# Kernel optimization log

Measured on AMD Instinct MI355X. Metric: run time of the kernel, lower is better.

The kernel has to match this reference:

```python
import jax, jax.numpy as jnp
import numpy as np

RESOLUTION = 0.1  # init arg `resolution`; hard=True -> hardtanh branch


def setup_inputs() -> dict:
    key = jax.random.key(0)
    B, L = 32, 1024  # documents x sentences per document
    score = jax.random.normal(key, (B * L,), dtype=jnp.float32)
    score_idx = jnp.arange(B * L, dtype=jnp.int32).reshape(B, L)
    return {"score": score, "score_idx": score_idx}


def _toeplitz(s):
    # Equivalent of pad_score: rows i = n-1 .. 1 of concat(zeros(n), s)
    # score_hat[r, j] = s[j - 1 - r] if j - 1 - r >= 0 else 0
    n = s.shape[0]
    r = jnp.arange(n - 1)[:, None]
    j = jnp.arange(n)[None, :]
    idx = j - 1 - r
    return jnp.where(idx >= 0, s[jnp.clip(idx, 0)], jnp.zeros((), s.dtype))


def _prob(score_hat, s):
    # hard=True: (hardtanh((hat - s)/res * 2 + 1) + 1) / 2
    z = (score_hat - s[None, :]) / RESOLUTION * 2.0 + 1.0
    return (jnp.clip(z, -1.0, 1.0) + 1.0) * 0.5


def _gate(s_doc):
    s = s_doc[1:-1]  # drop first/last sentence scores, length n = L-2
    fwd = jnp.cumprod(_prob(_toeplitz(s), s), axis=0)   # [n-1, n]
    sb = s[::-1]
    bwd = jnp.cumprod(_prob(_toeplitz(sb), sb), axis=0)  # [n-1, n]
    return jnp.stack([fwd, bwd], axis=0)  # [2, n-1, n]


def reference(score, score_idx):
    docs = score[score_idx]          # [B, L] gather per score_idx
    return jax.vmap(_gate)(docs)     # [B, 2, L-3, L-2]
```

## Files before the change

### kernel.cpp

```cpp
#include <hip/hip_runtime.h>

#define TPB   128
#define LSEQ  1024
#define NCOL  1022
#define NROW  1021
#define NPAD  1021
#define SLDS  (NPAD + NCOL)

__global__ __launch_bounds__(TPB) void gate_kernel(
    const float* __restrict__ score,
    const int*   __restrict__ score_idx,
    float*       __restrict__ out)
{
    __shared__ float sp[SLDS];

    const int bid = blockIdx.x;
    const int cb  = bid & 7;
    const int bd  = bid >> 3;
    const int d   = bd & 1;
    const int b   = bd >> 1;
    const int tid = threadIdx.x;

    for (int i = tid; i < NPAD; i += TPB) sp[i] = 0.0f;
    const int* idxRow = score_idx + b * LSEQ + 1;
    for (int i = tid; i < NCOL; i += TPB) {
        int src = (d == 0) ? i : (NCOL - 1 - i);
        sp[NPAD + i] = score[idxRow[src]];
    }
    __syncthreads();

    const int j = cb * TPB + tid;
    if (j >= NCOL) return;

    const float c = 1.0f - 10.0f * sp[NPAD + j];
    float a = 1.0f;
    int   m = NPAD + j - 1;
    float* outp = out + (size_t)bd * NROW * NCOL + j;

#define ROW(X)                                                        \
    {   float p = fminf(fmaxf(__builtin_fmaf((X), 10.0f, c), 0.0f), 1.0f); \
        a *= p; *outp = a; outp += NCOL; }

    for (int bt = 0; bt < NROW / 8; ++bt) {
        float x0 = sp[m    ], x1 = sp[m - 1], x2 = sp[m - 2], x3 = sp[m - 3];
        float x4 = sp[m - 4], x5 = sp[m - 5], x6 = sp[m - 6], x7 = sp[m - 7];
        m -= 8;
        ROW(x0); ROW(x1); ROW(x2); ROW(x3);
        ROW(x4); ROW(x5); ROW(x6); ROW(x7);
    }
    {
        float x0 = sp[m], x1 = sp[m - 1], x2 = sp[m - 2], x3 = sp[m - 3];
        float x4 = sp[m - 4];
        ROW(x0); ROW(x1); ROW(x2); ROW(x3); ROW(x4);
    }
#undef ROW
}

extern "C" void kernel_launch(void* const* d_in, const int* in_sizes, int n_in,
                              void* d_out, int out_size, void* d_ws, size_t ws_size,
                              hipStream_t stream)
{
    const float* score = (const float*)d_in[0];
    const int*   sidx  = (const int*)d_in[1];
    float*       out   = (float*)d_out;

    const int B = in_sizes[0] / LSEQ;
    dim3 grid(B * 2 * 8), block(TPB);
    gate_kernel<<<grid, block, 0, stream>>>(score, sidx, out);
}
```

Before: 50.87 us.

## Split work by row chunks with two columns per thread and paired stores

Each block now covers all columns for a 128-row slice of the cumulative product, instead of 128 columns across all rows. Each thread handles two adjacent columns and stores both as one 8-byte vector, so a block writes whole contiguous rows. Every thread first recomputes the running product up to its chunk's starting row, which adds redundant ALU and LDS work that grows for later chunks. The aim is better store coalescing and vector width on this write-bound kernel.

```diff
diff --git a/kernel.cpp b/kernel.cpp
--- a/kernel.cpp
+++ b/kernel.cpp
@@ -1,11 +1,15 @@
 #include <hip/hip_runtime.h>
 
-#define TPB   128
-#define LSEQ  1024
-#define NCOL  1022
-#define NROW  1021
-#define NPAD  1021
-#define SLDS  (NPAD + NCOL)
+#define TPB     512
+#define LSEQ    1024
+#define NCOL    1022
+#define NROW    1021
+#define NPAD    1021
+#define SLDS    (NPAD + NCOL)
+#define NCHUNK  8
+#define RPC     128
+
+typedef float v2f __attribute__((ext_vector_type(2)));
 
 __global__ __launch_bounds__(TPB) void gate_kernel(
     const float* __restrict__ score,
@@ -14,12 +18,12 @@
 {
     __shared__ float sp[SLDS];
 
-    const int bid = blockIdx.x;
-    const int cb  = bid & 7;
-    const int bd  = bid >> 3;
-    const int d   = bd & 1;
-    const int b   = bd >> 1;
-    const int tid = threadIdx.x;
+    const int bid   = blockIdx.x;
+    const int chunk = bid & (NCHUNK - 1);
+    const int bd    = bid >> 3;
+    const int d     = bd & 1;
+    const int b     = bd >> 1;
+    const int tid   = threadIdx.x;
 
     for (int i = tid; i < NPAD; i += TPB) sp[i] = 0.0f;
     const int* idxRow = score_idx + b * LSEQ + 1;
@@ -29,31 +33,54 @@
     }
     __syncthreads();
 
-    const int j = cb * TPB + tid;
-    if (j >= NCOL) return;
+    const int j0 = tid * 2;
+    if (j0 >= NCOL) return;
 
-    const float c = 1.0f - 10.0f * sp[NPAD + j];
-    float a = 1.0f;
-    int   m = NPAD + j - 1;
-    float* outp = out + (size_t)bd * NROW * NCOL + j;
+    const float c0 = 1.0f - 10.0f * sp[NPAD + j0];
+    const float c1 = 1.0f - 10.0f * sp[NPAD + j0 + 1];
 
-#define ROW(X)                                                        \
-    {   float p = fminf(fmaxf(__builtin_fmaf((X), 10.0f, c), 0.0f), 1.0f); \
-        a *= p; *outp = a; outp += NCOL; }
+    float a0 = 1.0f, a1 = 1.0f;
+    float vhi = sp[NPAD + j0];
+    int   m   = NPAD + j0 - 1;
 
-    for (int bt = 0; bt < NROW / 8; ++bt) {
+    const int r0 = chunk * RPC;
+    const int r1 = (r0 + RPC < NROW) ? r0 + RPC : NROW;
+
+#define STEP(X)                                                             \
+    {   float _v = (X);                                                     \
+        float _p0 = fminf(fmaxf(__builtin_fmaf(_v,  10.0f, c0), 0.0f), 1.0f); \
+        float _p1 = fminf(fmaxf(__builtin_fmaf(vhi, 10.0f, c1), 0.0f), 1.0f); \
+        a0 *= _p0; a1 *= _p1; vhi = _v; }
+
+    #pragma unroll 1
+    for (int bt = 0; bt < r0 / 8; ++bt) {
         float x0 = sp[m    ], x1 = sp[m - 1], x2 = sp[m - 2], x3 = sp[m - 3];
         float x4 = sp[m - 4], x5 = sp[m - 5], x6 = sp[m - 6], x7 = sp[m - 7];
         m -= 8;
-        ROW(x0); ROW(x1); ROW(x2); ROW(x3);
-        ROW(x4); ROW(x5); ROW(x6); ROW(x7);
+        STEP(x0); STEP(x1); STEP(x2); STEP(x3);
+        STEP(x4); STEP(x5); STEP(x6); STEP(x7);
     }
-    {
-        float x0 = sp[m], x1 = sp[m - 1], x2 = sp[m - 2], x3 = sp[m - 3];
-        float x4 = sp[m - 4];
-        ROW(x0); ROW(x1); ROW(x2); ROW(x3); ROW(x4);
+
+    float* outp = out + (size_t)bd * NROW * NCOL + (size_t)r0 * NCOL + j0;
+    const int nrows = r1 - r0;
+
+#define EMIT  { v2f w; w.x = a0; w.y = a1; *(v2f*)outp = w; outp += NCOL; }
+
+    #pragma unroll 1
+    for (int bt = 0; bt < nrows / 8; ++bt) {
+        float x0 = sp[m    ], x1 = sp[m - 1], x2 = sp[m - 2], x3 = sp[m - 3];
+        float x4 = sp[m - 4], x5 = sp[m - 5], x6 = sp[m - 6], x7 = sp[m - 7];
+        m -= 8;
+        STEP(x0); EMIT; STEP(x1); EMIT; STEP(x2); EMIT; STEP(x3); EMIT;
+        STEP(x4); EMIT; STEP(x5); EMIT; STEP(x6); EMIT; STEP(x7); EMIT;
     }
-#undef ROW
+    #pragma unroll 1
+    for (int r = nrows & ~7; r < nrows; ++r) {
+        float x = sp[m]; --m;
+        STEP(x); EMIT;
+    }
+#undef STEP
+#undef EMIT
 }
 
 extern "C" void kernel_launch(void* const* d_in, const int* in_sizes, int n_in,
@@ -65,6 +92,6 @@
     float*       out   = (float*)d_out;
 
     const int B = in_sizes[0] / LSEQ;
-    dim3 grid(B * 2 * 8), block(TPB);
+    dim3 grid(B * 2 * NCHUNK), block(TPB);
     gate_kernel<<<grid, block, 0, stream>>>(score, sidx, out);
 }
```

Measured after the change: 57.56 us. +13.1%, slower.
